# Kernel optimization log

Hardware: AMD Instinct MI355X
Metric: run time of the kernel (lower is better)

The kernel has to match this reference:

```python
import jax, jax.numpy as jnp
import numpy as np

B, S, E, H = 32, 4096, 256, 8
P, M = 256, 16  # positions per batch row, tokens per position (pileup depth)


def setup_inputs() -> dict:
    key = jax.random.key(0)
    k1, k2, k3, k4, k5, k6 = jax.random.split(key, 6)
    embeddings = jax.random.normal(k1, (B, S, E), jnp.float32)
    # each position 0..P-1 appears exactly M times per batch row, shuffled
    base = jnp.repeat(jnp.arange(P, dtype=jnp.int32), M)  # (S,)
    positions = jax.vmap(lambda k: jax.random.permutation(k, base))(jax.random.split(k2, B))
    scale = 1.0 / np.sqrt(E)
    Wq = jax.random.normal(k3, (E, E), jnp.float32) * scale
    Wk = jax.random.normal(k4, (E, E), jnp.float32) * scale
    Wv = jax.random.normal(k5, (E, E), jnp.float32) * scale
    W0 = jax.random.normal(k6, (E, E), jnp.float32) * scale
    return {"embeddings": embeddings, "Wq": Wq, "Wk": Wk, "Wv": Wv, "W0": W0,
            "positions": positions, "num_positions": P, "group_size": M, "num_heads": H}


def _intra_group_rank(positions):
    # rank[b,i] = number of earlier tokens j<i in row b with the same position
    Bb, Ss = positions.shape
    idx = jnp.arange(Ss)
    order = jnp.argsort(positions, axis=1)  # stable sort preserves original order within a group
    sp = jnp.take_along_axis(positions, order, axis=1)
    new_group = jnp.concatenate([jnp.ones((Bb, 1), bool), sp[:, 1:] != sp[:, :-1]], axis=1)
    group_start = jax.lax.cummax(jnp.where(new_group, idx[None, :], 0), axis=1)
    rank_sorted = idx[None, :] - group_start
    rank = jnp.zeros_like(positions).at[jnp.arange(Bb)[:, None], order].set(rank_sorted.astype(positions.dtype))
    return rank


def reference(embeddings, Wq, Wk, Wv, W0, positions, num_positions, group_size, num_heads):
    Bb, Ss, Ee = embeddings.shape
    Pp, Mm, Hh = num_positions, group_size, num_heads
    dh = Ee // Hh
    G = Bb * Pp

    valid = positions >= 0
    rank = _intra_group_rank(positions)                       # (B,S) slot within group
    gid = jnp.arange(Bb, dtype=positions.dtype)[:, None] * Pp + jnp.clip(positions, 0)  # (B,S)
    gid_scat = jnp.where(valid, gid, G)                        # out-of-bounds -> dropped

    # gather: ragged regroup into (G, M, E), zero-padded like the torch version
    grouped = jnp.zeros((G, Mm, Ee), embeddings.dtype).at[gid_scat, rank].set(embeddings, mode='drop')

    # multi-head self-attention within each group (no mask, matching the original)
    q = (grouped @ Wq).reshape(G, Mm, Hh, dh)
    k = (grouped @ Wk).reshape(G, Mm, Hh, dh)
    v = (grouped @ Wv).reshape(G, Mm, Hh, dh)
    scores = jnp.einsum('gmhd,gnhd->ghmn', q, k) / np.sqrt(dh).astype(embeddings.dtype)
    attn = jax.nn.softmax(scores, axis=-1)
    ctx = jnp.einsum('ghmn,gnhd->gmhd', attn, v).reshape(G, Mm, Ee)
    att_out = ctx @ W0                                         # (G, M, E)

    # scatter back; invalid (-1) slots stay zero, as in the torch loop
    out = jnp.where(valid[:, :, None], att_out[gid, rank], 0.0)
    return out
```

## Files before the change

### kernel.cpp

```cpp
#include <hip/hip_runtime.h>
#include <stdint.h>

#define B_    32
#define S_    4096
#define E_    256
#define P_    256
#define M_    16
#define G_    (B_*P_)
#define NSLOT (G_*M_)
#define GPW   8
#define ROWS  128
#define NWG   (G_/GPW)

typedef float fv4 __attribute__((ext_vector_type(4)));
typedef int   iv4 __attribute__((ext_vector_type(4)));
typedef int   iv2 __attribute__((ext_vector_type(2)));
typedef __bf16 bv8 __attribute__((ext_vector_type(8)));
typedef short  sv4 __attribute__((ext_vector_type(4)));

__device__ __forceinline__ uint32_t bf16rne(float f) {
  uint32_t u = __builtin_bit_cast(uint32_t, f);
  u += 0x7fffu + ((u >> 16) & 1u);
  return u >> 16;
}
__device__ __forceinline__ uint32_t pk2(uint32_t lo, uint32_t hi) {
  return (lo & 0xffffu) | (hi << 16);
}
__device__ __forceinline__ void mfma32(fv4& d, iv4 a, iv4 b) {
  d = __builtin_amdgcn_mfma_f32_16x16x32_bf16(
        __builtin_bit_cast(bv8, a), __builtin_bit_cast(bv8, b), d, 0, 0, 0);
}
__device__ __forceinline__ void mfma16(fv4& d, iv2 a, iv2 b) {
  d = __builtin_amdgcn_mfma_f32_16x16x16bf16_1k(
        __builtin_bit_cast(sv4, a), __builtin_bit_cast(sv4, b), d, 0, 0, 0);
}
__device__ __forceinline__ void gload_lds16(const void* g, void* l) {
  __builtin_amdgcn_global_load_lds(
      (const __attribute__((address_space(1))) uint32_t*)g,
      (__attribute__((address_space(3))) uint32_t*)l, 16, 0, 0);
}

#define SWZ(off, row) ((off) ^ (((row) & 7) << 4))
#define LQKV(row, cb) ( ((row) >> 1) * 128 + \
    (((((row) & 1) << 6) + (cb)) ^ ((((row) >> 1) & 7) << 4)) )

#define BAR()   { asm volatile("" ::: "memory"); __builtin_amdgcn_s_barrier(); \
                  asm volatile("" ::: "memory"); }
#define VMWAIT1 asm volatile("s_waitcnt vmcnt(1)" ::: "memory")
#define VMWAIT0 asm volatile("s_waitcnt vmcnt(0)" ::: "memory")
#define LGKM0   asm volatile("s_waitcnt lgkmcnt(0)" ::: "memory")

__global__ void k_init(int* cnt, int* s2t) {
  int i = blockIdx.x * 256 + threadIdx.x;
  if (i < G_) cnt[i] = 0;
  if (i < NSLOT) s2t[i] = -1;
}

__global__ void k_trans(const float* __restrict__ Wq, const float* __restrict__ Wk,
                        const float* __restrict__ Wv, const float* __restrict__ W0,
                        uint16_t* __restrict__ WT) {
  int o = blockIdx.x * 256 + threadIdx.x;
  int wsel = blockIdx.y;
  const float* W = (wsel == 0) ? Wq : (wsel == 1) ? Wk : (wsel == 2) ? Wv : W0;
  int n = o >> 8, k = o & 255;
  WT[(size_t)wsel * 65536 + o] = (uint16_t)bf16rne(W[k * 256 + n]);
}

__global__ void k_rank(const int* __restrict__ pos, int* cnt, int* s2t) {
  int i = blockIdx.x * 256 + threadIdx.x;
  if (i >= B_ * S_) return;
  int p = pos[i];
  if (p < 0 || p >= P_) return;
  int b = i >> 12;
  int g = (b << 8) + p;
  int r = atomicAdd(&cnt[g], 1);
  if (r < M_) s2t[g * M_ + r] = i;
}

__device__ __forceinline__ void stage_qkv(const uint16_t* Wt, int c0, char* buf,
                                          int w, int l) {
  int n = w * 2 + (l >> 5);
  int seg = l & 31;
  gload_lds16(reinterpret_cast<const char*>(Wt) + (size_t)(c0 + n) * 512 + SWZ(seg * 16, n),
              buf + w * 1024);
}
__device__ __forceinline__ void stage_w0(const uint16_t* W0T, int c0, char* buf,
                                         int w, int l) {
  int pair = w * 8 + (l >> 3);
  int jp = ((l & 7) * 16) ^ ((pair & 7) << 4);
  int n = 2 * pair + (jp >> 6);
  gload_lds16(reinterpret_cast<const char*>(W0T) + (size_t)n * 512 + c0 * 2 + (jp & 63),
              buf + w * 1024);
}

__global__ __launch_bounds__(1024, 1) void k_main(
    const float* __restrict__ emb, const int* __restrict__ s2t,
    const uint16_t* __restrict__ WT, float* __restrict__ out) {
  extern __shared__ char smem[];
  char* bufA = smem;
  char* bufB = smem + 16384;
  char* Qb = smem + 32768;
  char* Kb = smem + 40960;
  char* Vb = smem + 49152;
  char* Cb = smem + 57344;

  const uint16_t* WqT = WT;
  const uint16_t* WkT = WT + 65536;
  const uint16_t* WvT = WT + 131072;
  const uint16_t* W0T = WT + 196608;

  const int tid = threadIdx.x;
  const int l = tid & 63;
  const int w = tid >> 6;
  const int lane15 = l & 15;
  const int lq = l >> 4;
  const int rb = w >> 1;
  const int ch = w & 1;
  const int slot0 = blockIdx.x * ROWS;

  #pragma unroll 2
  for (int rl = 0; rl < 8; ++rl) {
    int row = w * 8 + rl;
    int t = s2t[slot0 + row];
    uint32_t u0 = 0, u1 = 0;
    if (t >= 0) {
      const float4 v = *reinterpret_cast<const float4*>(emb + (size_t)t * E_ + (l << 2));
      u0 = pk2(bf16rne(v.x), bf16rne(v.y));
      u1 = pk2(bf16rne(v.z), bf16rne(v.w));
    }
    iv2 val; val[0] = (int)u0; val[1] = (int)u1;
    *reinterpret_cast<iv2*>(smem + row * 512 + SWZ(l * 8, row)) = val;
  }
  __syncthreads();

  iv4 xf[8];
  const int arow = rb * 16 + lane15;
  #pragma unroll
  for (int ks = 0; ks < 8; ++ks)
    xf[ks] = *reinterpret_cast<const iv4*>(smem + arow * 512 + SWZ(ks * 64 + lq * 16, arow));
  __syncthreads();

  fv4 outacc[8];
  #pragma unroll
  for (int i = 0; i < 8; ++i) outacc[i] = fv4{0.f, 0.f, 0.f, 0.f};

  stage_qkv(WqT, 0, bufA, w, l);
  stage_qkv(WkT, 0, bufB, w, l);

  for (int hc = 0; hc < 8; ++hc) {
    const int c0 = hc * 32;

    #define COMPUTE_QKV(buf, dst)                                            \
    {                                                                        \
      fv4 a0 = fv4{0.f,0.f,0.f,0.f};                                         \
      const int n0 = ch * 16 + lane15;                                       \
      _Pragma("unroll")                                                      \
      for (int ks = 0; ks < 8; ++ks) {                                       \
        iv4 b0 = *reinterpret_cast<const iv4*>((buf) + n0 * 512 + SWZ(ks * 64 + lq * 16, n0)); \
        mfma32(a0, xf[ks], b0);                                              \
      }                                                                      \
      _Pragma("unroll")                                                      \
      for (int r = 0; r < 4; ++r) {                                          \
        int row = rb * 16 + lq * 4 + r;                                      \
        *reinterpret_cast<uint16_t*>((dst) + LQKV(row, n0 * 2)) =            \
            (uint16_t)bf16rne(a0[r]);                                        \
      }                                                                      \
    }

    VMWAIT1; BAR();
    COMPUTE_QKV(bufA, Qb);
    LGKM0; BAR();
    stage_qkv(WvT, c0, bufA, w, l);

    VMWAIT1; BAR();
    COMPUTE_QKV(bufB, Kb);
    LGKM0; BAR();
    stage_w0(W0T, c0, bufB, w, l);

    VMWAIT1; BAR();
    COMPUTE_QKV(bufA, Vb);
    LGKM0; BAR();
    if (hc < 7) stage_qkv(WqT, c0 + 32, bufA, w, l);

    {
      const int frow = rb * 16 + lane15;
      iv4 kf = *reinterpret_cast<const iv4*>(Kb + LQKV(frow, lq * 16));
      iv4 qf = *reinterpret_cast<const iv4*>(Qb + LQKV(frow, lq * 16));
      fv4 s = fv4{0.f, 0.f, 0.f, 0.f};
      mfma32(s, kf, qf);
      float mx = fmaxf(fmaxf(s[0], s[1]), fmaxf(s[2], s[3]));
      mx = fmaxf(mx, __shfl_xor(mx, 16));
      mx = fmaxf(mx, __shfl_xor(mx, 32));
      const float Cc = 0.25503373f;
      float e0 = exp2f((s[0] - mx) * Cc), e1 = exp2f((s[1] - mx) * Cc);
      float e2 = exp2f((s[2] - mx) * Cc), e3 = exp2f((s[3] - mx) * Cc);
      float sum = e0 + e1 + e2 + e3;
      sum += __shfl_xor(sum, 16);
      sum += __shfl_xor(sum, 32);
      float inv = 1.0f / sum;
      iv2 pa; pa[0] = (int)pk2(bf16rne(e0 * inv), bf16rne(e1 * inv));
              pa[1] = (int)pk2(bf16rne(e2 * inv), bf16rne(e3 * inv));
      const int r0 = rb * 16 + lq * 4;
      const int cb = (ch * 16 + lane15) * 2;
      uint32_t v0 = *reinterpret_cast<const uint16_t*>(Vb + LQKV(r0 + 0, cb));
      uint32_t v1 = *reinterpret_cast<const uint16_t*>(Vb + LQKV(r0 + 1, cb));
      uint32_t v2 = *reinterpret_cast<const uint16_t*>(Vb + LQKV(r0 + 2, cb));
      uint32_t v3 = *reinterpret_cast<const uint16_t*>(Vb + LQKV(r0 + 3, cb));
      iv2 bv; bv[0] = (int)pk2(v0, v1); bv[1] = (int)pk2(v2, v3);
      fv4 cacc = fv4{0.f, 0.f, 0.f, 0.f};
      mfma16(cacc, pa, bv);
      #pragma unroll
      for (int r = 0; r < 4; ++r)
        *reinterpret_cast<uint16_t*>(Cb + LQKV(r0 + r, cb)) =
            (uint16_t)bf16rne(cacc[r]);
    }

    if (hc < 7) { VMWAIT1; } else { VMWAIT0; }
    LGKM0; BAR();
    {
      int ar = rb * 16 + lane15;
      iv4 af = *reinterpret_cast<const iv4*>(Cb + LQKV(ar, lq * 16));
      #pragma unroll
      for (int nt = 0; nt < 8; ++nt) {
        int n = ch * 128 + nt * 16 + lane15;
        iv4 bfg = *reinterpret_cast<const iv4*>(
            bufB + (n >> 1) * 128 + ((((n & 1) << 6) + lq * 16) ^ (((n >> 1) & 7) << 4)));
        mfma32(outacc[nt], af, bfg);
      }
    }
    BAR();
    if (hc < 7) stage_qkv(WkT, c0 + 32, bufB, w, l);
    #undef COMPUTE_QKV
  }

  #pragma unroll
  for (int r = 0; r < 4; ++r) {
    int t = s2t[slot0 + rb * 16 + lq * 4 + r];
    if (t < 0) continue;
    #pragma unroll
    for (int nt = 0; nt < 8; ++nt) {
      int col = ch * 128 + nt * 16 + lane15;
      out[(size_t)t * E_ + col] = outacc[nt][r];
    }
  }
}

extern "C" void kernel_launch(void* const* d_in, const int* in_sizes, int n_in,
                              void* d_out, int out_size, void* d_ws, size_t ws_size,
                              hipStream_t stream) {
  (void)in_sizes; (void)n_in; (void)out_size; (void)ws_size;
  const float* emb = (const float*)d_in[0];
  const float* Wq  = (const float*)d_in[1];
  const float* Wk  = (const float*)d_in[2];
  const float* Wv  = (const float*)d_in[3];
  const float* W0  = (const float*)d_in[4];
  const int*   pos = (const int*)d_in[5];
  float* out = (float*)d_out;

  int* cnt = (int*)d_ws;
  int* s2t = (int*)((char*)d_ws + 32768);
  uint16_t* WT = (uint16_t*)((char*)d_ws + 32768 + 524288);

  (void)hipFuncSetAttribute(reinterpret_cast<const void*>(k_main),
                            hipFuncAttributeMaxDynamicSharedMemorySize, 65536);

  k_init <<<512, 256, 0, stream>>>(cnt, s2t);
  k_trans<<<dim3(256, 4), 256, 0, stream>>>(Wq, Wk, Wv, W0, WT);
  k_rank <<<512, 256, 0, stream>>>(pos, cnt, s2t);
  k_main <<<NWG, 1024, 65536, stream>>>(emb, s2t, WT, out);
}
```

Baseline: 177.4 us.

## Process two heads per pipeline stage with doubled weight tiles in LDS

Each loop iteration now handles 64 weight columns (two heads) instead of 32, halving the iteration count and the number of barriers and pipeline stages. Staging buffers and Q/K/V/C tiles double in size, so LDS grows to 128KB and the wait counts move to vmcnt(2). The QKV matmul issues two MFMA chains per k-step for more ILP, and the attention/context and W0 stages are reorganised so each wave pair handles one head. The trade-off is higher LDS use and a different swizzled layout. The launch-bounds min-blocks hint is also dropped.

```diff
diff --git a/kernel.cpp b/kernel.cpp
--- a/kernel.cpp
+++ b/kernel.cpp
@@ -41,12 +41,11 @@
 }
 
 #define SWZ(off, row) ((off) ^ (((row) & 7) << 4))
-#define LQKV(row, cb) ( ((row) >> 1) * 128 + \
-    (((((row) & 1) << 6) + (cb)) ^ ((((row) >> 1) & 7) << 4)) )
+#define LQ(row, cb) ((row) * 128 + ((cb) ^ (((row) & 7) << 4)))
 
 #define BAR()   { asm volatile("" ::: "memory"); __builtin_amdgcn_s_barrier(); \
                   asm volatile("" ::: "memory"); }
-#define VMWAIT1 asm volatile("s_waitcnt vmcnt(1)" ::: "memory")
+#define VMWAIT2 asm volatile("s_waitcnt vmcnt(2)" ::: "memory")
 #define VMWAIT0 asm volatile("s_waitcnt vmcnt(0)" ::: "memory")
 #define LGKM0   asm volatile("s_waitcnt lgkmcnt(0)" ::: "memory")
 
@@ -79,30 +78,37 @@
 
 __device__ __forceinline__ void stage_qkv(const uint16_t* Wt, int c0, char* buf,
                                           int w, int l) {
-  int n = w * 2 + (l >> 5);
-  int seg = l & 31;
-  gload_lds16(reinterpret_cast<const char*>(Wt) + (size_t)(c0 + n) * 512 + SWZ(seg * 16, n),
-              buf + w * 1024);
+  #pragma unroll
+  for (int it = 0; it < 2; ++it) {
+    int q = it * 16 + w;
+    int n = q * 2 + (l >> 5);
+    int seg = l & 31;
+    gload_lds16(reinterpret_cast<const char*>(Wt) + (size_t)(c0 + n) * 512 + SWZ(seg * 16, n),
+                buf + q * 1024);
+  }
 }
 __device__ __forceinline__ void stage_w0(const uint16_t* W0T, int c0, char* buf,
                                          int w, int l) {
-  int pair = w * 8 + (l >> 3);
-  int jp = ((l & 7) * 16) ^ ((pair & 7) << 4);
-  int n = 2 * pair + (jp >> 6);
-  gload_lds16(reinterpret_cast<const char*>(W0T) + (size_t)n * 512 + c0 * 2 + (jp & 63),
-              buf + w * 1024);
-}
-
-__global__ __launch_bounds__(1024, 1) void k_main(
+  #pragma unroll
+  for (int it = 0; it < 2; ++it) {
+    int q = it * 16 + w;
+    int n = q * 8 + (l >> 3);
+    int off = (l & 7) * 16;
+    gload_lds16(reinterpret_cast<const char*>(W0T) + (size_t)n * 512 + c0 * 2 + (off ^ ((n & 7) << 4)),
+                buf + q * 1024);
+  }
+}
+
+__global__ __launch_bounds__(1024) void k_main(
     const float* __restrict__ emb, const int* __restrict__ s2t,
     const uint16_t* __restrict__ WT, float* __restrict__ out) {
   extern __shared__ char smem[];
   char* bufA = smem;
-  char* bufB = smem + 16384;
-  char* Qb = smem + 32768;
-  char* Kb = smem + 40960;
-  char* Vb = smem + 49152;
-  char* Cb = smem + 57344;
+  char* bufB = smem + 32768;
+  char* Qb = smem + 65536;
+  char* Kb = smem + 81920;
+  char* Vb = smem + 98304;
+  char* Cb = smem + 114688;
 
   const uint16_t* WqT = WT;
   const uint16_t* WkT = WT + 65536;
@@ -147,45 +153,50 @@
   stage_qkv(WqT, 0, bufA, w, l);
   stage_qkv(WkT, 0, bufB, w, l);
 
-  for (int hc = 0; hc < 8; ++hc) {
-    const int c0 = hc * 32;
+  for (int hc = 0; hc < 4; ++hc) {
+    const int c0 = hc * 64;
 
     #define COMPUTE_QKV(buf, dst)                                            \
     {                                                                        \
-      fv4 a0 = fv4{0.f,0.f,0.f,0.f};                                         \
-      const int n0 = ch * 16 + lane15;                                       \
+      fv4 a0 = fv4{0.f,0.f,0.f,0.f}, a1 = fv4{0.f,0.f,0.f,0.f};              \
+      const int n0 = ch * 32 + lane15, n1 = ch * 32 + lane15 + 16;           \
       _Pragma("unroll")                                                      \
       for (int ks = 0; ks < 8; ++ks) {                                       \
         iv4 b0 = *reinterpret_cast<const iv4*>((buf) + n0 * 512 + SWZ(ks * 64 + lq * 16, n0)); \
+        iv4 b1 = *reinterpret_cast<const iv4*>((buf) + n1 * 512 + SWZ(ks * 64 + lq * 16, n1)); \
         mfma32(a0, xf[ks], b0);                                              \
+        mfma32(a1, xf[ks], b1);                                              \
       }                                                                      \
       _Pragma("unroll")                                                      \
       for (int r = 0; r < 4; ++r) {                                          \
         int row = rb * 16 + lq * 4 + r;                                      \
-        *reinterpret_cast<uint16_t*>((dst) + LQKV(row, n0 * 2)) =            \
+        *reinterpret_cast<uint16_t*>((dst) + LQ(row, n0 * 2)) =              \
             (uint16_t)bf16rne(a0[r]);                                        \
+        *reinterpret_cast<uint16_t*>((dst) + LQ(row, n1 * 2)) =              \
+            (uint16_t)bf16rne(a1[r]);                                        \
       }                                                                      \
     }
 
-    VMWAIT1; BAR();
+    VMWAIT2; BAR();
     COMPUTE_QKV(bufA, Qb);
     LGKM0; BAR();
     stage_qkv(WvT, c0, bufA, w, l);
 
-    VMWAIT1; BAR();
+    VMWAIT2; BAR();
     COMPUTE_QKV(bufB, Kb);
     LGKM0; BAR();
     stage_w0(W0T, c0, bufB, w, l);
 
-    VMWAIT1; BAR();
+    VMWAIT2; BAR();
     COMPUTE_QKV(bufA, Vb);
     LGKM0; BAR();
-    if (hc < 7) stage_qkv(WqT, c0 + 32, bufA, w, l);
+    if (hc < 3) stage_qkv(WqT, c0 + 64, bufA, w, l);
 
     {
-      const int frow = rb * 16 + lane15;
-      iv4 kf = *reinterpret_cast<const iv4*>(Kb + LQKV(frow, lq * 16));
-      iv4 qf = *reinterpret_cast<const iv4*>(Qb + LQKV(frow, lq * 16));
+      const int g = w >> 1, hh = w & 1;
+      const int frow = g * 16 + lane15;
+      iv4 kf = *reinterpret_cast<const iv4*>(Kb + LQ(frow, hh * 64 + lq * 16));
+      iv4 qf = *reinterpret_cast<const iv4*>(Qb + LQ(frow, hh * 64 + lq * 16));
       fv4 s = fv4{0.f, 0.f, 0.f, 0.f};
       mfma32(s, kf, qf);
       float mx = fmaxf(fmaxf(s[0], s[1]), fmaxf(s[2], s[3]));
@@ -200,36 +211,40 @@
       float inv = 1.0f / sum;
       iv2 pa; pa[0] = (int)pk2(bf16rne(e0 * inv), bf16rne(e1 * inv));
               pa[1] = (int)pk2(bf16rne(e2 * inv), bf16rne(e3 * inv));
-      const int r0 = rb * 16 + lq * 4;
-      const int cb = (ch * 16 + lane15) * 2;
-      uint32_t v0 = *reinterpret_cast<const uint16_t*>(Vb + LQKV(r0 + 0, cb));
-      uint32_t v1 = *reinterpret_cast<const uint16_t*>(Vb + LQKV(r0 + 1, cb));
-      uint32_t v2 = *reinterpret_cast<const uint16_t*>(Vb + LQKV(r0 + 2, cb));
-      uint32_t v3 = *reinterpret_cast<const uint16_t*>(Vb + LQKV(r0 + 3, cb));
-      iv2 bv; bv[0] = (int)pk2(v0, v1); bv[1] = (int)pk2(v2, v3);
-      fv4 cacc = fv4{0.f, 0.f, 0.f, 0.f};
-      mfma16(cacc, pa, bv);
+      const int r0 = g * 16 + lq * 4;
       #pragma unroll
-      for (int r = 0; r < 4; ++r)
-        *reinterpret_cast<uint16_t*>(Cb + LQKV(r0 + r, cb)) =
-            (uint16_t)bf16rne(cacc[r]);
-    }
-
-    if (hc < 7) { VMWAIT1; } else { VMWAIT0; }
-    LGKM0; BAR();
-    {
+      for (int dvt = 0; dvt < 2; ++dvt) {
+        int cb = (hh * 32 + dvt * 16 + lane15) * 2;
+        uint32_t v0 = *reinterpret_cast<const uint16_t*>(Vb + LQ(r0 + 0, cb));
+        uint32_t v1 = *reinterpret_cast<const uint16_t*>(Vb + LQ(r0 + 1, cb));
+        uint32_t v2 = *reinterpret_cast<const uint16_t*>(Vb + LQ(r0 + 2, cb));
+        uint32_t v3 = *reinterpret_cast<const uint16_t*>(Vb + LQ(r0 + 3, cb));
+        iv2 bv; bv[0] = (int)pk2(v0, v1); bv[1] = (int)pk2(v2, v3);
+        fv4 cacc = fv4{0.f, 0.f, 0.f, 0.f};
+        mfma16(cacc, pa, bv);
+        #pragma unroll
+        for (int r = 0; r < 4; ++r)
+          *reinterpret_cast<uint16_t*>(Cb + LQ(r0 + r, cb)) =
+              (uint16_t)bf16rne(cacc[r]);
+      }
+    }
+
+    if (hc < 3) { VMWAIT2; } else { VMWAIT0; }
+    LGKM0; BAR();
+    #pragma unroll
+    for (int ks = 0; ks < 2; ++ks) {
       int ar = rb * 16 + lane15;
-      iv4 af = *reinterpret_cast<const iv4*>(Cb + LQKV(ar, lq * 16));
+      iv4 af = *reinterpret_cast<const iv4*>(Cb + LQ(ar, ks * 64 + lq * 16));
       #pragma unroll
       for (int nt = 0; nt < 8; ++nt) {
         int n = ch * 128 + nt * 16 + lane15;
         iv4 bfg = *reinterpret_cast<const iv4*>(
-            bufB + (n >> 1) * 128 + ((((n & 1) << 6) + lq * 16) ^ (((n >> 1) & 7) << 4)));
+            bufB + n * 128 + ((ks * 64 + lq * 16) ^ ((n & 7) << 4)));
         mfma32(outacc[nt], af, bfg);
       }
     }
     BAR();
-    if (hc < 7) stage_qkv(WkT, c0 + 32, bufB, w, l);
+    if (hc < 3) stage_qkv(WkT, c0 + 64, bufB, w, l);
     #undef COMPUTE_QKV
   }
 
@@ -262,10 +277,10 @@
   uint16_t* WT = (uint16_t*)((char*)d_ws + 32768 + 524288);
 
   (void)hipFuncSetAttribute(reinterpret_cast<const void*>(k_main),
-                            hipFuncAttributeMaxDynamicSharedMemorySize, 65536);
+                            hipFuncAttributeMaxDynamicSharedMemorySize, 131072);
 
   k_init <<<512, 256, 0, stream>>>(cnt, s2t);
   k_trans<<<dim3(256, 4), 256, 0, stream>>>(Wq, Wk, Wv, W0, WT);
   k_rank <<<512, 256, 0, stream>>>(pos, cnt, s2t);
-  k_main <<<NWG, 1024, 65536, stream>>>(emb, s2t, WT, out);
-}
+  k_main <<<NWG, 1024, 131072, stream>>>(emb, s2t, WT, out);
+}
```

After: 252.6 us. 42.4% more time.

## Double-buffer whole Q/K/V weight sets and give W0 its own LDS buffer

Applied to the files above, without the earlier changes.

The main kernel's weight staging now uses two full Q/K/V weight sets in LDS plus a dedicated W0 buffer. All three next-chunk Q/K/V slices are prefetched at once while the current chunk is computed. This removes most of the per-chunk barriers and the serialized single-buffer ping-pong that made each projection wait on its own load. The cost is growing dynamic LDS from 64 KB to 144 KB and dropping the explicit min-blocks launch bound, which leaves even less LDS headroom per CU.

```diff
diff --git a/kernel.cpp b/kernel.cpp
--- a/kernel.cpp
+++ b/kernel.cpp
@@ -46,7 +46,7 @@
 
 #define BAR()   { asm volatile("" ::: "memory"); __builtin_amdgcn_s_barrier(); \
                   asm volatile("" ::: "memory"); }
-#define VMWAIT1 asm volatile("s_waitcnt vmcnt(1)" ::: "memory")
+#define VMWAIT3 asm volatile("s_waitcnt vmcnt(3)" ::: "memory")
 #define VMWAIT0 asm volatile("s_waitcnt vmcnt(0)" ::: "memory")
 #define LGKM0   asm volatile("s_waitcnt lgkmcnt(0)" ::: "memory")
 
@@ -93,16 +93,17 @@
               buf + w * 1024);
 }
 
-__global__ __launch_bounds__(1024, 1) void k_main(
+__global__ __launch_bounds__(1024) void k_main(
     const float* __restrict__ emb, const int* __restrict__ s2t,
     const uint16_t* __restrict__ WT, float* __restrict__ out) {
   extern __shared__ char smem[];
-  char* bufA = smem;
-  char* bufB = smem + 16384;
-  char* Qb = smem + 32768;
-  char* Kb = smem + 40960;
-  char* Vb = smem + 49152;
-  char* Cb = smem + 57344;
+  char* set0 = smem;
+  char* set1 = smem + 49152;
+  char* w0b  = smem + 98304;
+  char* Qb = smem + 114688;
+  char* Kb = smem + 122880;
+  char* Vb = smem + 131072;
+  char* Cb = smem + 139264;
 
   const uint16_t* WqT = WT;
   const uint16_t* WkT = WT + 65536;
@@ -144,11 +145,14 @@
   #pragma unroll
   for (int i = 0; i < 8; ++i) outacc[i] = fv4{0.f, 0.f, 0.f, 0.f};
 
-  stage_qkv(WqT, 0, bufA, w, l);
-  stage_qkv(WkT, 0, bufB, w, l);
+  stage_qkv(WqT, 0, set0,         w, l);
+  stage_qkv(WkT, 0, set0 + 16384, w, l);
+  stage_qkv(WvT, 0, set0 + 32768, w, l);
 
   for (int hc = 0; hc < 8; ++hc) {
     const int c0 = hc * 32;
+    char* sc = (hc & 1) ? set1 : set0;
+    char* sn = (hc & 1) ? set0 : set1;
 
     #define COMPUTE_QKV(buf, dst)                                            \
     {                                                                        \
@@ -167,23 +171,23 @@
       }                                                                      \
     }
 
-    VMWAIT1; BAR();
-    COMPUTE_QKV(bufA, Qb);
-    LGKM0; BAR();
-    stage_qkv(WvT, c0, bufA, w, l);
-
-    VMWAIT1; BAR();
-    COMPUTE_QKV(bufB, Kb);
-    LGKM0; BAR();
-    stage_w0(W0T, c0, bufB, w, l);
-
-    VMWAIT1; BAR();
-    COMPUTE_QKV(bufA, Vb);
-    LGKM0; BAR();
-    if (hc < 7) stage_qkv(WqT, c0 + 32, bufA, w, l);
-
+    VMWAIT0;
+    BAR();
+    stage_w0(W0T, c0, w0b, w, l);
+    if (hc < 7) {
+      stage_qkv(WqT, c0 + 32, sn,         w, l);
+      stage_qkv(WkT, c0 + 32, sn + 16384, w, l);
+      stage_qkv(WvT, c0 + 32, sn + 32768, w, l);
+    }
+    COMPUTE_QKV(sc,         Qb);
+    COMPUTE_QKV(sc + 16384, Kb);
+    COMPUTE_QKV(sc + 32768, Vb);
+    LGKM0;
+
+    BAR();
     {
-      const int frow = rb * 16 + lane15;
+      const int g = w >> 1;
+      const int frow = g * 16 + lane15;
       iv4 kf = *reinterpret_cast<const iv4*>(Kb + LQKV(frow, lq * 16));
       iv4 qf = *reinterpret_cast<const iv4*>(Qb + LQKV(frow, lq * 16));
       fv4 s = fv4{0.f, 0.f, 0.f, 0.f};
@@ -200,7 +204,7 @@
       float inv = 1.0f / sum;
       iv2 pa; pa[0] = (int)pk2(bf16rne(e0 * inv), bf16rne(e1 * inv));
               pa[1] = (int)pk2(bf16rne(e2 * inv), bf16rne(e3 * inv));
-      const int r0 = rb * 16 + lq * 4;
+      const int r0 = g * 16 + lq * 4;
       const int cb = (ch * 16 + lane15) * 2;
       uint32_t v0 = *reinterpret_cast<const uint16_t*>(Vb + LQKV(r0 + 0, cb));
       uint32_t v1 = *reinterpret_cast<const uint16_t*>(Vb + LQKV(r0 + 1, cb));
@@ -214,9 +218,10 @@
         *reinterpret_cast<uint16_t*>(Cb + LQKV(r0 + r, cb)) =
             (uint16_t)bf16rne(cacc[r]);
     }
-
-    if (hc < 7) { VMWAIT1; } else { VMWAIT0; }
-    LGKM0; BAR();
+    LGKM0;
+
+    if (hc < 7) { VMWAIT3; } else { VMWAIT0; }
+    BAR();
     {
       int ar = rb * 16 + lane15;
       iv4 af = *reinterpret_cast<const iv4*>(Cb + LQKV(ar, lq * 16));
@@ -224,12 +229,11 @@
       for (int nt = 0; nt < 8; ++nt) {
         int n = ch * 128 + nt * 16 + lane15;
         iv4 bfg = *reinterpret_cast<const iv4*>(
-            bufB + (n >> 1) * 128 + ((((n & 1) << 6) + lq * 16) ^ (((n >> 1) & 7) << 4)));
+            w0b + (n >> 1) * 128 + ((((n & 1) << 6) + lq * 16) ^ (((n >> 1) & 7) << 4)));
         mfma32(outacc[nt], af, bfg);
       }
     }
-    BAR();
-    if (hc < 7) stage_qkv(WkT, c0 + 32, bufB, w, l);
+    LGKM0;
     #undef COMPUTE_QKV
   }
 
@@ -262,10 +266,10 @@
   uint16_t* WT = (uint16_t*)((char*)d_ws + 32768 + 524288);
 
   (void)hipFuncSetAttribute(reinterpret_cast<const void*>(k_main),
-                            hipFuncAttributeMaxDynamicSharedMemorySize, 65536);
+                            hipFuncAttributeMaxDynamicSharedMemorySize, 147456);
 
   k_init <<<512, 256, 0, stream>>>(cnt, s2t);
   k_trans<<<dim3(256, 4), 256, 0, stream>>>(Wq, Wk, Wv, W0, WT);
   k_rank <<<512, 256, 0, stream>>>(pos, cnt, s2t);
-  k_main <<<NWG, 1024, 65536, stream>>>(emb, s2t, WT, out);
-}
+  k_main <<<NWG, 1024, 147456, stream>>>(emb, s2t, WT, out);
+}
```

New measurement: 200.3 us. 1.13x slower.

## Halve workgroup size and run two workgroups per CU, reading X from LDS

Applied to the files above, without the earlier changes.

Each workgroup now handles 4 groups (64 rows) with 512 threads instead of 8 groups with 1024 threads, and launch bounds allow two workgroups per CU. The embedding tile stays in LDS and is re-read for every QKV MFMA instead of being held in registers, which lowers register pressure. Each wave now issues two weight-staging loads per stage, so the vmcnt waits are adjusted to match. The aim is to let two independent workgroups overlap their barriers and load latency. The cost is twice as many weight-tile loads from L2 overall, extra LDS reads, and 80 KB of LDS per workgroup.

```diff
diff --git a/kernel.cpp b/kernel.cpp
--- a/kernel.cpp
+++ b/kernel.cpp
@@ -8,8 +8,8 @@
 #define M_    16
 #define G_    (B_*P_)
 #define NSLOT (G_*M_)
-#define GPW   8
-#define ROWS  128
+#define GPW   4
+#define ROWS  64
 #define NWG   (G_/GPW)
 
 typedef float fv4 __attribute__((ext_vector_type(4)));
@@ -46,7 +46,7 @@
 
 #define BAR()   { asm volatile("" ::: "memory"); __builtin_amdgcn_s_barrier(); \
                   asm volatile("" ::: "memory"); }
-#define VMWAIT1 asm volatile("s_waitcnt vmcnt(1)" ::: "memory")
+#define VMWAIT2 asm volatile("s_waitcnt vmcnt(2)" ::: "memory")
 #define VMWAIT0 asm volatile("s_waitcnt vmcnt(0)" ::: "memory")
 #define LGKM0   asm volatile("s_waitcnt lgkmcnt(0)" ::: "memory")
 
@@ -79,30 +79,39 @@
 
 __device__ __forceinline__ void stage_qkv(const uint16_t* Wt, int c0, char* buf,
                                           int w, int l) {
-  int n = w * 2 + (l >> 5);
-  int seg = l & 31;
-  gload_lds16(reinterpret_cast<const char*>(Wt) + (size_t)(c0 + n) * 512 + SWZ(seg * 16, n),
-              buf + w * 1024);
+  #pragma unroll
+  for (int it = 0; it < 2; ++it) {
+    int q = it * 8 + w;
+    int n = q * 2 + (l >> 5);
+    int seg = l & 31;
+    gload_lds16(reinterpret_cast<const char*>(Wt) + (size_t)(c0 + n) * 512 + SWZ(seg * 16, n),
+                buf + q * 1024);
+  }
 }
 __device__ __forceinline__ void stage_w0(const uint16_t* W0T, int c0, char* buf,
                                          int w, int l) {
-  int pair = w * 8 + (l >> 3);
-  int jp = ((l & 7) * 16) ^ ((pair & 7) << 4);
-  int n = 2 * pair + (jp >> 6);
-  gload_lds16(reinterpret_cast<const char*>(W0T) + (size_t)n * 512 + c0 * 2 + (jp & 63),
-              buf + w * 1024);
-}
-
-__global__ __launch_bounds__(1024, 1) void k_main(
+  #pragma unroll
+  for (int it = 0; it < 2; ++it) {
+    int q = it * 8 + w;
+    int pair = q * 8 + (l >> 3);
+    int jp = ((l & 7) * 16) ^ ((pair & 7) << 4);
+    int n = 2 * pair + (jp >> 6);
+    gload_lds16(reinterpret_cast<const char*>(W0T) + (size_t)n * 512 + c0 * 2 + (jp & 63),
+                buf + q * 1024);
+  }
+}
+
+__global__ __launch_bounds__(512, 2) void k_main(
     const float* __restrict__ emb, const int* __restrict__ s2t,
     const uint16_t* __restrict__ WT, float* __restrict__ out) {
   extern __shared__ char smem[];
-  char* bufA = smem;
-  char* bufB = smem + 16384;
-  char* Qb = smem + 32768;
-  char* Kb = smem + 40960;
-  char* Vb = smem + 49152;
-  char* Cb = smem + 57344;
+  char* Xb   = smem;
+  char* bufA = smem + 32768;
+  char* bufB = smem + 49152;
+  char* Qb = smem + 65536;
+  char* Kb = smem + 69632;
+  char* Vb = smem + 73728;
+  char* Cb = smem + 77824;
 
   const uint16_t* WqT = WT;
   const uint16_t* WkT = WT + 65536;
@@ -129,15 +138,8 @@
       u1 = pk2(bf16rne(v.z), bf16rne(v.w));
     }
     iv2 val; val[0] = (int)u0; val[1] = (int)u1;
-    *reinterpret_cast<iv2*>(smem + row * 512 + SWZ(l * 8, row)) = val;
-  }
-  __syncthreads();
-
-  iv4 xf[8];
-  const int arow = rb * 16 + lane15;
-  #pragma unroll
-  for (int ks = 0; ks < 8; ++ks)
-    xf[ks] = *reinterpret_cast<const iv4*>(smem + arow * 512 + SWZ(ks * 64 + lq * 16, arow));
+    *reinterpret_cast<iv2*>(Xb + row * 512 + SWZ(l * 8, row)) = val;
+  }
   __syncthreads();
 
   fv4 outacc[8];
@@ -154,10 +156,12 @@
     {                                                                        \
       fv4 a0 = fv4{0.f,0.f,0.f,0.f};                                         \
       const int n0 = ch * 16 + lane15;                                       \
+      const int ar2 = rb * 16 + lane15;                                      \
       _Pragma("unroll")                                                      \
       for (int ks = 0; ks < 8; ++ks) {                                       \
+        iv4 av = *reinterpret_cast<const iv4*>(Xb + ar2 * 512 + SWZ(ks * 64 + lq * 16, ar2)); \
         iv4 b0 = *reinterpret_cast<const iv4*>((buf) + n0 * 512 + SWZ(ks * 64 + lq * 16, n0)); \
-        mfma32(a0, xf[ks], b0);                                              \
+        mfma32(a0, av, b0);                                                  \
       }                                                                      \
       _Pragma("unroll")                                                      \
       for (int r = 0; r < 4; ++r) {                                          \
@@ -167,17 +171,17 @@
       }                                                                      \
     }
 
-    VMWAIT1; BAR();
+    VMWAIT2; BAR();
     COMPUTE_QKV(bufA, Qb);
     LGKM0; BAR();
     stage_qkv(WvT, c0, bufA, w, l);
 
-    VMWAIT1; BAR();
+    VMWAIT2; BAR();
     COMPUTE_QKV(bufB, Kb);
     LGKM0; BAR();
     stage_w0(W0T, c0, bufB, w, l);
 
-    VMWAIT1; BAR();
+    VMWAIT2; BAR();
     COMPUTE_QKV(bufA, Vb);
     LGKM0; BAR();
     if (hc < 7) stage_qkv(WqT, c0 + 32, bufA, w, l);
@@ -215,7 +219,7 @@
             (uint16_t)bf16rne(cacc[r]);
     }
 
-    if (hc < 7) { VMWAIT1; } else { VMWAIT0; }
+    if (hc < 7) { VMWAIT2; } else { VMWAIT0; }
     LGKM0; BAR();
     {
       int ar = rb * 16 + lane15;
@@ -262,10 +266,10 @@
   uint16_t* WT = (uint16_t*)((char*)d_ws + 32768 + 524288);
 
   (void)hipFuncSetAttribute(reinterpret_cast<const void*>(k_main),
-                            hipFuncAttributeMaxDynamicSharedMemorySize, 65536);
+                            hipFuncAttributeMaxDynamicSharedMemorySize, 81920);
 
   k_init <<<512, 256, 0, stream>>>(cnt, s2t);
   k_trans<<<dim3(256, 4), 256, 0, stream>>>(Wq, Wk, Wv, W0, WT);
   k_rank <<<512, 256, 0, stream>>>(pos, cnt, s2t);
-  k_main <<<NWG, 1024, 65536, stream>>>(emb, s2t, WT, out);
-}
+  k_main <<<NWG, 512, 81920, stream>>>(emb, s2t, WT, out);
+}
```

New measurement: 254.5 us. 43.5% more time.
